# Kernel tuning notes

Measured on AMD Instinct MI355X. Metric: run time of the kernel, lower is better.

## Reference

```python
import jax, jax.numpy as jnp
import numpy as np

# ProjectorConfig defaults
MIN_SPEECH_FRAMES = 1.0
MAX_SPEECH_EXPAND = 3.0
TAIL_HOLD_UNITS = 2
BOUNDARY_COMMIT_THRESHOLD = 0.45

B, U = 4096, 2048


def setup_inputs() -> dict:
    key = jax.random.key(0)
    ks = jax.random.split(key, 10)
    # ragged prefix mask: random visible length per row (faithful to streaming use)
    lengths = jax.random.randint(ks[0], (B,), 1, U + 1)
    unit_mask = (jnp.arange(U)[None, :] < lengths[:, None]).astype(jnp.float32)
    dur_anchor_src = jax.random.uniform(ks[1], (B, U), jnp.float32) * 20.0
    dur_logratio_unit = jax.random.normal(ks[2], (B, U), jnp.float32) * 0.3
    pause_weight_unit = jax.random.uniform(ks[3], (B, U), jnp.float32)
    boundary_latent = jax.random.uniform(ks[4], (B, U), jnp.float32)
    speech_budget_win = jax.random.uniform(ks[5], (B, 1), jnp.float32) * float(U) * 10.0
    pause_budget_win = jax.random.uniform(ks[6], (B, 1), jnp.float32) * float(U)
    open_run_mask = jax.random.bernoulli(ks[7], 0.1, (B, U)).astype(jnp.int32)
    return {
        "dur_anchor_src": dur_anchor_src,
        "unit_mask": unit_mask,
        "speech_budget_win": speech_budget_win,
        "pause_budget_win": pause_budget_win,
        "dur_logratio_unit": dur_logratio_unit,
        "pause_weight_unit": pause_weight_unit,
        "boundary_latent": boundary_latent,
        "phase_ptr": jnp.zeros((B,), jnp.float32),
        "backlog": jnp.zeros((B,), jnp.float32),
        "clock_delta": jnp.zeros((B,), jnp.float32),
        "commit_frontier": jnp.zeros((B,), jnp.int32),
        "open_run_mask": open_run_mask,
    }


def reference(dur_anchor_src, unit_mask, speech_budget_win, pause_budget_win,
              dur_logratio_unit, pause_weight_unit, boundary_latent,
              phase_ptr, backlog, clock_delta, commit_frontier, open_run_mask):
    b, u = unit_mask.shape

    # ---- _project_speech ----
    anchor = jnp.maximum(dur_anchor_src, MIN_SPEECH_FRAMES)
    base = anchor * jnp.exp(dur_logratio_unit)
    speech = jnp.maximum(jnp.minimum(base, anchor * MAX_SPEECH_EXPAND), MIN_SPEECH_FRAMES) * unit_mask
    total = jnp.maximum((speech * unit_mask).sum(axis=1, keepdims=True), 1e-6)
    speech = speech * (speech_budget_win / total) * unit_mask

    # ---- _project_pause ----
    scores = jnp.maximum(pause_weight_unit, 0.0) * (0.5 + boundary_latent) * unit_mask
    score_total = scores.sum(axis=1, keepdims=True)
    fallback = unit_mask / jnp.maximum(unit_mask.sum(axis=1, keepdims=True), 1.0)
    weights = jnp.where(score_total > 0, scores / jnp.maximum(score_total, 1e-6), fallback)
    pause = weights * pause_budget_win

    effective = (speech + pause) * unit_mask

    # ---- _compute_commit_frontier (vectorized) ----
    visible = unit_mask.sum(axis=1).astype(jnp.int32)                 # active_len [B]
    idx = jnp.arange(u, dtype=jnp.int32)[None, :]
    open_vis = (open_run_mask > 0) & (idx < visible[:, None])
    has_open = open_vis.any(axis=1)
    first_open = jnp.argmax(open_vis, axis=1).astype(jnp.int32)
    closed_prefix = jnp.where(has_open, first_open, visible)          # leading closed run
    release_cap = jnp.maximum(visible - TAIL_HOLD_UNITS, 0)
    candidate = jnp.minimum(release_cap, closed_prefix)
    prev = commit_frontier.astype(jnp.int32)
    b_idx = jnp.clip(candidate - 1, 0, u - 1)
    b_val = jnp.take_along_axis(boundary_latent, b_idx[:, None], axis=1)[:, 0]
    soft = (candidate > 0) & (candidate < visible) & (b_val < BOUNDARY_COMMIT_THRESHOLD)
    candidate = jnp.where(soft, jnp.maximum(prev, candidate - 1), candidate)
    commit = jnp.maximum(prev, candidate)

    # ---- _advance_state (prefix sums instead of python loops) ----
    zeros_col = jnp.zeros((b, 1), effective.dtype)
    cs_eff = jnp.concatenate([zeros_col, jnp.cumsum(effective, axis=1)], axis=1)
    cs_src = jnp.concatenate([zeros_col, jnp.cumsum(dur_anchor_src, axis=1)], axis=1)
    take = lambda cs, i: jnp.take_along_axis(cs, i[:, None], axis=1)[:, 0]
    exec_prefix = take(cs_eff, commit) - take(cs_eff, prev)
    src_prefix = take(cs_src, commit) - take(cs_src, prev)
    adv = commit > prev
    delta = exec_prefix - src_prefix
    next_clock = jnp.where(adv, clock_delta + delta, clock_delta)
    next_backlog = jnp.where(adv, jnp.maximum(next_clock, 0.0), backlog)
    visible_total = jnp.maximum(effective.sum(axis=1), 1.0)
    next_phase = jnp.where(adv, jnp.clip(phase_ptr + exec_prefix / visible_total, 0.0, 1.0), phase_ptr)

    return (speech, pause, effective, commit, next_phase, next_backlog, next_clock)
```

## Files before the change

kernel.cpp:

```cpp
#include <hip/hip_runtime.h>
#include <climits>


constexpr int UNITS = 2048;
constexpr int BLOCK = 256;

static __device__ __forceinline__ float waveSum(float v) {
#pragma unroll
  for (int off = 32; off > 0; off >>= 1) v += __shfl_down(v, off, 64);
  return v;
}
static __device__ __forceinline__ int waveMin(int v) {
#pragma unroll
  for (int off = 32; off > 0; off >>= 1) v = min(v, __shfl_down(v, off, 64));
  return v;
}

__global__ __launch_bounds__(BLOCK) void rhythm_kernel(
    const float* __restrict__ dur_anchor,
    const float* __restrict__ unit_mask,
    const float* __restrict__ speech_budget,
    const float* __restrict__ pause_budget,
    const float* __restrict__ dur_logratio,
    const float* __restrict__ pause_weight,
    const float* __restrict__ boundary,
    const float* __restrict__ phase_ptr,
    const float* __restrict__ backlog,
    const float* __restrict__ clock_delta,
    const int*   __restrict__ commit_front,
    const int*   __restrict__ open_run,
    float* __restrict__ out,
    int B) {
  const int row = blockIdx.x;
  const int t = threadIdx.x;
  const size_t base = (size_t)row * UNITS;

  float sv_src[8];
  float sv_sr[8];
  float sv_sc[8];
  float sv_m[8];

  float sum_sr = 0.f, sum_sc = 0.f, sum_m = 0.f;
  int min_open = INT_MAX;

#pragma unroll
  for (int c = 0; c < 2; ++c) {
    const int e0 = c * 1024 + 4 * t;
    const float4 a4 = *(const float4*)(dur_anchor  + base + e0);
    const float4 m4 = *(const float4*)(unit_mask   + base + e0);
    const float4 l4 = *(const float4*)(dur_logratio + base + e0);
    const float4 p4 = *(const float4*)(pause_weight + base + e0);
    const float4 b4 = *(const float4*)(boundary     + base + e0);
    const int4   o4 = *(const int4*)(open_run      + base + e0);
    const float av[4] = {a4.x, a4.y, a4.z, a4.w};
    const float mv[4] = {m4.x, m4.y, m4.z, m4.w};
    const float lv[4] = {l4.x, l4.y, l4.z, l4.w};
    const float pv[4] = {p4.x, p4.y, p4.z, p4.w};
    const float bv[4] = {b4.x, b4.y, b4.z, b4.w};
    const int   ov[4] = {o4.x, o4.y, o4.z, o4.w};
#pragma unroll
    for (int j = 0; j < 4; ++j) {
      const int k = c * 4 + j;
      const float m = mv[j];
      const float a = fmaxf(av[j], 1.0f);
      const float bse = a * __expf(lv[j]);
      const float sr = fmaxf(fminf(bse, 3.0f * a), 1.0f) * m;
      const float sc = fmaxf(pv[j], 0.0f) * (0.5f + bv[j]) * m;
      sv_src[k] = av[j];
      sv_sr[k] = sr;
      sv_sc[k] = sc;
      sv_m[k] = m;
      sum_sr += sr;
      sum_sc += sc;
      sum_m += m;
      if (ov[j] > 0 && m > 0.5f) min_open = min(min_open, e0 + j);
    }
  }

  const int wv = t >> 6, ln = t & 63;
  __shared__ float sf[3][4];
  __shared__ int si[4];
  __shared__ float sh_sscale, sh_pscale, sh_fb;
  __shared__ int sh_commit, sh_prev, sh_usefb;

  const float r0 = waveSum(sum_sr);
  const float r1 = waveSum(sum_sc);
  const float r2 = waveSum(sum_m);
  const int ri = waveMin(min_open);
  if (ln == 0) { sf[0][wv] = r0; sf[1][wv] = r1; sf[2][wv] = r2; si[wv] = ri; }
  __syncthreads();

  if (t == 0) {
    const float ts = sf[0][0] + sf[0][1] + sf[0][2] + sf[0][3];
    const float tc = sf[1][0] + sf[1][1] + sf[1][2] + sf[1][3];
    const float tm = sf[2][0] + sf[2][1] + sf[2][2] + sf[2][3];
    const int mo = min(min(si[0], si[1]), min(si[2], si[3]));

    const int visible = (int)(tm + 0.5f);
    const int closed = (mo == INT_MAX) ? visible : mo;
    const int relcap = max(visible - 2, 0);
    int cand = min(relcap, closed);
    const int prev = commit_front[row];
    const int bidx = min(max(cand - 1, 0), UNITS - 1);
    const float bval = boundary[base + bidx];
    if (cand > 0 && cand < visible && bval < 0.45f)
      cand = max(prev, cand - 1);
    sh_commit = max(prev, cand);
    sh_prev = prev;

    sh_sscale = speech_budget[row] / fmaxf(ts, 1e-6f);
    const float pb = pause_budget[row];
    if (tc > 0.0f) {
      sh_usefb = 0; sh_pscale = pb / fmaxf(tc, 1e-6f); sh_fb = 0.f;
    } else {
      sh_usefb = 1; sh_pscale = 0.f; sh_fb = pb / fmaxf(tm, 1.0f);
    }
  }
  __syncthreads();

  const float sscale = sh_sscale;
  const float pscale = sh_pscale;
  const float fb = sh_fb;
  const int usefb = sh_usefb;
  const int commit = sh_commit;
  const int prev = sh_prev;

  float* __restrict__ out_speech = out;
  float* __restrict__ out_pause  = out + (size_t)B * UNITS;
  float* __restrict__ out_eff    = out + 2 * (size_t)B * UNITS;

  float eff_rng = 0.f, src_rng = 0.f, eff_tot = 0.f;
#pragma unroll
  for (int c = 0; c < 2; ++c) {
    const int e0 = c * 1024 + 4 * t;
    float s_[4], p_[4], e_[4];
#pragma unroll
    for (int j = 0; j < 4; ++j) {
      const int k = c * 4 + j;
      const int idx = e0 + j;
      const float m = sv_m[k];
      const float speech = sv_sr[k] * sscale;
      const float pause = usefb ? (m * fb) : (sv_sc[k] * pscale);
      const float eff = (speech + pause) * m;
      s_[j] = speech;
      p_[j] = pause;
      e_[j] = eff;
      eff_tot += eff;
      const bool inr = (idx >= prev) && (idx < commit);
      eff_rng += inr ? eff : 0.f;
      src_rng += inr ? sv_src[k] : 0.f;
    }
    *reinterpret_cast<float4*>(out_speech + base + e0) =
        make_float4(s_[0], s_[1], s_[2], s_[3]);
    *reinterpret_cast<float4*>(out_pause + base + e0) =
        make_float4(p_[0], p_[1], p_[2], p_[3]);
    *reinterpret_cast<float4*>(out_eff + base + e0) =
        make_float4(e_[0], e_[1], e_[2], e_[3]);
  }

  const float q0 = waveSum(eff_rng);
  const float q1 = waveSum(src_rng);
  const float q2 = waveSum(eff_tot);
  if (ln == 0) { sf[0][wv] = q0; sf[1][wv] = q1; sf[2][wv] = q2; }
  __syncthreads();

  if (t == 0) {
    const float execp = sf[0][0] + sf[0][1] + sf[0][2] + sf[0][3];
    const float srcp  = sf[1][0] + sf[1][1] + sf[1][2] + sf[1][3];
    const float etot  = sf[2][0] + sf[2][1] + sf[2][2] + sf[2][3];
    const bool adv = commit > prev;
    const float cd = clock_delta[row];
    const float nclock = adv ? (cd + (execp - srcp)) : cd;
    const float nback = adv ? fmaxf(nclock, 0.0f) : backlog[row];
    const float vt = fmaxf(etot, 1.0f);
    const float nphase =
        adv ? fminf(fmaxf(phase_ptr[row] + execp / vt, 0.0f), 1.0f) : phase_ptr[row];
    const size_t o = 3 * (size_t)B * UNITS;
    out[o + row] = (float)commit;
    out[o + (size_t)B + row] = nphase;
    out[o + 2 * (size_t)B + row] = nback;
    out[o + 3 * (size_t)B + row] = nclock;
  }
}

extern "C" void kernel_launch(void* const* d_in, const int* in_sizes, int n_in,
                              void* d_out, int out_size, void* d_ws, size_t ws_size,
                              hipStream_t stream) {
  const int B = in_sizes[7];
  rhythm_kernel<<<dim3(B), dim3(BLOCK), 0, stream>>>(
      (const float*)d_in[0],
      (const float*)d_in[1],
      (const float*)d_in[2],
      (const float*)d_in[3],
      (const float*)d_in[4],
      (const float*)d_in[5],
      (const float*)d_in[6],
      (const float*)d_in[7],
      (const float*)d_in[8],
      (const float*)d_in[9],
      (const int*)d_in[10],
      (const int*)d_in[11],
      (float*)d_out, B);
}
```

Baseline: 268.7 us.

## Process each row with a single wavefront and drop shared-memory reductions

```diff
diff --git a/kernel.cpp b/kernel.cpp
--- a/kernel.cpp
+++ b/kernel.cpp
@@ -3,20 +3,21 @@
 
 
 constexpr int UNITS = 2048;
-constexpr int BLOCK = 256;
+constexpr int BLOCK = 64;
+constexpr int CH = UNITS / (BLOCK * 4);
 
-static __device__ __forceinline__ float waveSum(float v) {
+static __device__ __forceinline__ float bflySum(float v) {
 #pragma unroll
-  for (int off = 32; off > 0; off >>= 1) v += __shfl_down(v, off, 64);
+  for (int m = 1; m < 64; m <<= 1) v += __shfl_xor(v, m, 64);
   return v;
 }
-static __device__ __forceinline__ int waveMin(int v) {
+static __device__ __forceinline__ int bflyMin(int v) {
 #pragma unroll
-  for (int off = 32; off > 0; off >>= 1) v = min(v, __shfl_down(v, off, 64));
+  for (int m = 1; m < 64; m <<= 1) v = min(v, __shfl_xor(v, m, 64));
   return v;
 }
 
-__global__ __launch_bounds__(BLOCK) void rhythm_kernel(
+__global__ __launch_bounds__(BLOCK, 4) void rhythm_kernel(
     const float* __restrict__ dur_anchor,
     const float* __restrict__ unit_mask,
     const float* __restrict__ speech_budget,
@@ -35,23 +36,27 @@
   const int t = threadIdx.x;
   const size_t base = (size_t)row * UNITS;
 
-  float sv_src[8];
-  float sv_sr[8];
-  float sv_sc[8];
-  float sv_m[8];
+  const int prev = commit_front[row];
+  const float sb = speech_budget[row];
+  const float pb = pause_budget[row];
+  const float pp = phase_ptr[row];
+  const float bl = backlog[row];
+  const float cd = clock_delta[row];
 
+  float sv_sr[CH * 4];
+  float sv_src[CH * 4];
   float sum_sr = 0.f, sum_sc = 0.f, sum_m = 0.f;
   int min_open = INT_MAX;
 
 #pragma unroll
-  for (int c = 0; c < 2; ++c) {
-    const int e0 = c * 1024 + 4 * t;
-    const float4 a4 = *(const float4*)(dur_anchor  + base + e0);
-    const float4 m4 = *(const float4*)(unit_mask   + base + e0);
+  for (int c = 0; c < CH; ++c) {
+    const int e0 = c * (BLOCK * 4) + 4 * t;
+    const float4 a4 = *(const float4*)(dur_anchor   + base + e0);
+    const float4 m4 = *(const float4*)(unit_mask    + base + e0);
     const float4 l4 = *(const float4*)(dur_logratio + base + e0);
     const float4 p4 = *(const float4*)(pause_weight + base + e0);
     const float4 b4 = *(const float4*)(boundary     + base + e0);
-    const int4   o4 = *(const int4*)(open_run      + base + e0);
+    const int4   o4 = *(const int4*)(open_run       + base + e0);
     const float av[4] = {a4.x, a4.y, a4.z, a4.w};
     const float mv[4] = {m4.x, m4.y, m4.z, m4.w};
     const float lv[4] = {l4.x, l4.y, l4.z, l4.w};
@@ -66,10 +71,8 @@
       const float bse = a * __expf(lv[j]);
       const float sr = fmaxf(fminf(bse, 3.0f * a), 1.0f) * m;
       const float sc = fmaxf(pv[j], 0.0f) * (0.5f + bv[j]) * m;
+      sv_sr[k] = sr;
       sv_src[k] = av[j];
-      sv_sr[k] = sr;
-      sv_sc[k] = sc;
-      sv_m[k] = m;
       sum_sr += sr;
       sum_sc += sc;
       sum_m += m;
@@ -77,53 +80,25 @@
     }
   }
 
-  const int wv = t >> 6, ln = t & 63;
-  __shared__ float sf[3][4];
-  __shared__ int si[4];
-  __shared__ float sh_sscale, sh_pscale, sh_fb;
-  __shared__ int sh_commit, sh_prev, sh_usefb;
+  const float ts = bflySum(sum_sr);
+  const float tc = bflySum(sum_sc);
+  const float tm = bflySum(sum_m);
+  const int mo = bflyMin(min_open);
 
-  const float r0 = waveSum(sum_sr);
-  const float r1 = waveSum(sum_sc);
-  const float r2 = waveSum(sum_m);
-  const int ri = waveMin(min_open);
-  if (ln == 0) { sf[0][wv] = r0; sf[1][wv] = r1; sf[2][wv] = r2; si[wv] = ri; }
-  __syncthreads();
+  const int visible = (int)(tm + 0.5f);
+  const int closed = (mo == INT_MAX) ? visible : mo;
+  const int relcap = max(visible - 2, 0);
+  int cand = min(relcap, closed);
+  const int bidx = min(max(cand - 1, 0), UNITS - 1);
+  const float bval = boundary[base + bidx];
+  if (cand > 0 && cand < visible && bval < 0.45f)
+    cand = max(prev, cand - 1);
+  const int commit = max(prev, cand);
 
-  if (t == 0) {
-    const float ts = sf[0][0] + sf[0][1] + sf[0][2] + sf[0][3];
-    const float tc = sf[1][0] + sf[1][1] + sf[1][2] + sf[1][3];
-    const float tm = sf[2][0] + sf[2][1] + sf[2][2] + sf[2][3];
-    const int mo = min(min(si[0], si[1]), min(si[2], si[3]));
-
-    const int visible = (int)(tm + 0.5f);
-    const int closed = (mo == INT_MAX) ? visible : mo;
-    const int relcap = max(visible - 2, 0);
-    int cand = min(relcap, closed);
-    const int prev = commit_front[row];
-    const int bidx = min(max(cand - 1, 0), UNITS - 1);
-    const float bval = boundary[base + bidx];
-    if (cand > 0 && cand < visible && bval < 0.45f)
-      cand = max(prev, cand - 1);
-    sh_commit = max(prev, cand);
-    sh_prev = prev;
-
-    sh_sscale = speech_budget[row] / fmaxf(ts, 1e-6f);
-    const float pb = pause_budget[row];
-    if (tc > 0.0f) {
-      sh_usefb = 0; sh_pscale = pb / fmaxf(tc, 1e-6f); sh_fb = 0.f;
-    } else {
-      sh_usefb = 1; sh_pscale = 0.f; sh_fb = pb / fmaxf(tm, 1.0f);
-    }
-  }
-  __syncthreads();
-
-  const float sscale = sh_sscale;
-  const float pscale = sh_pscale;
-  const float fb = sh_fb;
-  const int usefb = sh_usefb;
-  const int commit = sh_commit;
-  const int prev = sh_prev;
+  const float sscale = sb / fmaxf(ts, 1e-6f);
+  const bool usefb = !(tc > 0.0f);
+  const float pscale = pb / fmaxf(tc, 1e-6f);
+  const float fbw = pb / fmaxf(tm, 1.0f);
 
   float* __restrict__ out_speech = out;
   float* __restrict__ out_pause  = out + (size_t)B * UNITS;
@@ -131,19 +106,25 @@
 
   float eff_rng = 0.f, src_rng = 0.f, eff_tot = 0.f;
 #pragma unroll
-  for (int c = 0; c < 2; ++c) {
-    const int e0 = c * 1024 + 4 * t;
-    float s_[4], p_[4], e_[4];
+  for (int c = 0; c < CH; ++c) {
+    const int e0 = c * (BLOCK * 4) + 4 * t;
+    const float4 p4 = *(const float4*)(pause_weight + base + e0);
+    const float4 b4 = *(const float4*)(boundary     + base + e0);
+    const float pv[4] = {p4.x, p4.y, p4.z, p4.w};
+    const float bv[4] = {b4.x, b4.y, b4.z, b4.w};
+    float s_[4], q_[4], e_[4];
 #pragma unroll
     for (int j = 0; j < 4; ++j) {
       const int k = c * 4 + j;
       const int idx = e0 + j;
-      const float m = sv_m[k];
-      const float speech = sv_sr[k] * sscale;
-      const float pause = usefb ? (m * fb) : (sv_sc[k] * pscale);
+      const float sr = sv_sr[k];
+      const float m = (sr != 0.0f) ? 1.0f : 0.0f;
+      const float sc = fmaxf(pv[j], 0.0f) * (0.5f + bv[j]) * m;
+      const float speech = sr * sscale;
+      const float pause = usefb ? (m * fbw) : (sc * pscale);
       const float eff = (speech + pause) * m;
       s_[j] = speech;
-      p_[j] = pause;
+      q_[j] = pause;
       e_[j] = eff;
       eff_tot += eff;
       const bool inr = (idx >= prev) && (idx < commit);
@@ -153,28 +134,22 @@
     *reinterpret_cast<float4*>(out_speech + base + e0) =
         make_float4(s_[0], s_[1], s_[2], s_[3]);
     *reinterpret_cast<float4*>(out_pause + base + e0) =
-        make_float4(p_[0], p_[1], p_[2], p_[3]);
+        make_float4(q_[0], q_[1], q_[2], q_[3]);
     *reinterpret_cast<float4*>(out_eff + base + e0) =
         make_float4(e_[0], e_[1], e_[2], e_[3]);
   }
 
-  const float q0 = waveSum(eff_rng);
-  const float q1 = waveSum(src_rng);
-  const float q2 = waveSum(eff_tot);
-  if (ln == 0) { sf[0][wv] = q0; sf[1][wv] = q1; sf[2][wv] = q2; }
-  __syncthreads();
+  const float execp = bflySum(eff_rng);
+  const float srcp = bflySum(src_rng);
+  const float etot = bflySum(eff_tot);
 
   if (t == 0) {
-    const float execp = sf[0][0] + sf[0][1] + sf[0][2] + sf[0][3];
-    const float srcp  = sf[1][0] + sf[1][1] + sf[1][2] + sf[1][3];
-    const float etot  = sf[2][0] + sf[2][1] + sf[2][2] + sf[2][3];
     const bool adv = commit > prev;
-    const float cd = clock_delta[row];
     const float nclock = adv ? (cd + (execp - srcp)) : cd;
-    const float nback = adv ? fmaxf(nclock, 0.0f) : backlog[row];
+    const float nback = adv ? fmaxf(nclock, 0.0f) : bl;
     const float vt = fmaxf(etot, 1.0f);
     const float nphase =
-        adv ? fminf(fmaxf(phase_ptr[row] + execp / vt, 0.0f), 1.0f) : phase_ptr[row];
+        adv ? fminf(fmaxf(pp + execp / vt, 0.0f), 1.0f) : pp;
     const size_t o = 3 * (size_t)B * UNITS;
     out[o + row] = (float)commit;
     out[o + (size_t)B + row] = nphase;
```

New measurement: 294.9 us. +9.8%, slower.
